# Kernel tuning notes

Hardware: AMD Instinct MI355X
Metric: run time of the kernel (lower is better)

The kernel has to match this reference:

```python
import jax, jax.numpy as jnp
import numpy as np


def setup_inputs() -> dict:
    key = jax.random.key(0)
    k1, k2, k3 = jax.random.split(key, 3)
    B, Cin, H, W = 64, 16, 256, 256
    Cout, K = 64, 3
    x = jax.random.normal(k1, (B, Cin, H, W), dtype=jnp.float32)
    # PyTorch Conv2d init scale ~ 1/sqrt(fan_in)
    fan_in = Cin * K * K
    conv_weight = jax.random.normal(k2, (Cout, Cin, K, K), dtype=jnp.float32) / np.sqrt(fan_in)
    conv_bias = jax.random.normal(k3, (Cout,), dtype=jnp.float32) / np.sqrt(fan_in)
    return {"x": x, "conv_weight": conv_weight, "conv_bias": conv_bias}


def reference(x, conv_weight, conv_bias):
    # Conv2d: stride=1, padding=0 (VALID), dilation=1, groups=1
    y = jax.lax.conv_general_dilated(
        x, conv_weight,
        window_strides=(1, 1),
        padding="VALID",
        dimension_numbers=("NCHW", "OIHW", "NCHW"),
    ) + conv_bias[None, :, None, None]          # [B, Cout, 254, 254]
    m = jnp.min(y, axis=1, keepdims=True)        # [B, 1, 254, 254] min over channels
    return jnp.tanh(jnp.tanh(m))                 # double tanh
```

## Files before the change

### kernel.cpp

```cpp
#include <hip/hip_runtime.h>
#include <math.h>

#define CIN    16
#define COUT   64
#define H      256
#define W      256
#define OH     254
#define OW     254
#define NTAP   9
#define RING   8
#define SROW   264
#define NIT    32

typedef _Float16 f16x8  __attribute__((ext_vector_type(8)));
typedef float    f32x16 __attribute__((ext_vector_type(16)));

#define XP(px) ((px) ^ (((px) >> 3) & 7))

__global__ void wpack_kernel(const float* __restrict__ w, _Float16* __restrict__ wpk) {
    int idx = blockIdx.x * 256 + threadIdx.x;
    if (idx >= NTAP * 2 * 64 * 8) return;
    int e = idx & 7, l = (idx >> 3) & 63, m = (idx >> 9) & 1, t = idx >> 10;
    int co  = (l & 31) + 32 * m;
    int cin = 8 * (l >> 5) + e;
    wpk[idx] = (_Float16)w[((co * CIN + cin) * 3 + t / 3) * 3 + (t % 3)];
}

__device__ __forceinline__ float tanh_fast(float v) {
    float e = __expf(2.0f * v);
    return 1.0f - 2.0f * __builtin_amdgcn_rcpf(e + 1.0f);
}
__device__ __forceinline__ float min3f(float a, float b, float c) {
    return fminf(fminf(a, b), c);
}

__global__ __launch_bounds__(256, 2) void conv_mfma_kernel(
        const float* __restrict__ x, const f16x8* __restrict__ wpk,
        const float* __restrict__ bias, float* __restrict__ out) {
    __shared__ f16x8 xs[RING * SROW];

    const int tid  = threadIdx.x;
    const int lane = tid & 63;

    int bid = blockIdx.x;
    int nb  = (bid & 7) * 64 + (bid >> 3);
    int b   = nb >> 3;
    int rem = nb & 7;
    const int P0 = (rem & 1) * 128;
    const int r0 = (rem >> 1) * 64;

    const float* xb = x + (size_t)b * CIN * H * W;

    f16x8 wreg[NTAP][2];
#pragma unroll
    for (int t = 0; t < NTAP; ++t)
#pragma unroll
        for (int m = 0; m < 2; ++m)
            wreg[t][m] = wpk[(t * 2 + m) * 64 + lane];

    const int wave = tid >> 6;
    const int l31  = lane & 31;
    const int g2   = lane >> 5;

    const int sr = tid >> 7;
    const int sg = (tid >> 6) & 1;
    const int sp = tid & 63;
    const bool hduty = (sp == 63);

    float2 vm[8];
    float2 vh[8];

#define SLOAD(dRel)                                                             \
    {                                                                           \
        int row_ = r0 + (dRel); if (row_ > 255) row_ = 255;                     \
        const float* p_ = xb + (size_t)row_ * W;                                \
        _Pragma("unroll")                                                       \
        for (int c = 0; c < 8; ++c)                                             \
            vm[c] = *(const float2*)(p_ + (size_t)(8 * sg + c) * (H * W) + P0 + 2 * sp); \
        if (hduty) {                                                            \
            int hp_ = P0 + 128; if (hp_ > 254) hp_ = 254;                       \
            _Pragma("unroll")                                                   \
            for (int c = 0; c < 8; ++c)                                         \
                vh[c] = *(const float2*)(p_ + (size_t)(8 * sg + c) * (H * W) + hp_); \
        }                                                                       \
    }

#define SWRITE(slot)                                                            \
    {                                                                           \
        f16x8 q0, q1;                                                           \
        _Pragma("unroll")                                                       \
        for (int c = 0; c < 8; ++c) { q0[c] = (_Float16)vm[c].x;                \
                                      q1[c] = (_Float16)vm[c].y; }              \
        f16x8* base_ = xs + (slot) * SROW + sg * 132;                           \
        base_[XP(2 * sp)]     = q0;                                             \
        base_[XP(2 * sp + 1)] = q1;                                             \
        if (hduty) {                                                            \
            f16x8 h0, h1;                                                       \
            _Pragma("unroll")                                                   \
            for (int c = 0; c < 8; ++c) { h0[c] = (_Float16)vh[c].x;            \
                                          h1[c] = (_Float16)vh[c].y; }          \
            base_[XP(128)] = h0;                                                \
            base_[XP(129)] = h1;                                                \
        }                                                                       \
    }

#pragma unroll
    for (int j = 0; j < 3; ++j) {
        SLOAD(2 * j + sr)
        SWRITE(2 * j + sr)
    }

    int roff[3];
#pragma unroll
    for (int kw = 0; kw < 3; ++kw)
        roff[kw] = g2 * 132 + XP(32 * wave + l31 + kw);

    f32x16 cbias[2];
#pragma unroll
    for (int m = 0; m < 2; ++m)
#pragma unroll
        for (int r = 0; r < 16; ++r)
            cbias[m][r] = bias[(r & 3) + 8 * (r >> 2) + 4 * g2 + 32 * m];

    __syncthreads();

#pragma unroll 1
    for (int i = 0; i < NIT; ++i) {
        const bool pf = (i < 30);
        if (pf) SLOAD(2 * i + 6 + sr)

        f32x16 acc[2][2];
#pragma unroll
        for (int dd = 0; dd < 4; ++dd) {
            const f16x8* xr = xs + ((2 * i + dd) & 7) * SROW;
            f16x8 f0 = xr[roff[0]];
            f16x8 f1 = xr[roff[1]];
            f16x8 f2 = xr[roff[2]];
#pragma unroll
            for (int ro = 0; ro < 2; ++ro) {
                const int kh = dd - ro;
                if (kh < 0 || kh > 2) continue;
#pragma unroll
                for (int m = 0; m < 2; ++m) {
                    if (kh == 0)
                        acc[ro][m] = __builtin_amdgcn_mfma_f32_32x32x16_f16(wreg[0][m], f0, cbias[m], 0, 0, 0);
                    else
                        acc[ro][m] = __builtin_amdgcn_mfma_f32_32x32x16_f16(wreg[kh * 3][m], f0, acc[ro][m], 0, 0, 0);
                    acc[ro][m] = __builtin_amdgcn_mfma_f32_32x32x16_f16(wreg[kh * 3 + 1][m], f1, acc[ro][m], 0, 0, 0);
                    acc[ro][m] = __builtin_amdgcn_mfma_f32_32x32x16_f16(wreg[kh * 3 + 2][m], f2, acc[ro][m], 0, 0, 0);
                }
            }
        }

        __syncthreads();
        if (pf) SWRITE((2 * i + 6 + sr) & 7)

#pragma unroll
        for (int ro = 0; ro < 2; ++ro) {
            const int oh = r0 + 2 * i + ro;
            float mn = fminf(acc[ro][0][0], acc[ro][1][0]);
#pragma unroll
            for (int q = 1; q < 16; ++q)
                mn = min3f(acc[ro][0][q], acc[ro][1][q], mn);
            mn = fminf(mn, __shfl_xor(mn, 32));
            float t2 = tanh_fast(tanh_fast(mn));
            const int px = P0 + 32 * wave + l31;
            if (g2 == 0 && px < OW && oh < OH)
                out[((size_t)b * OH + oh) * OW + px] = t2;
        }
    }
}

extern "C" void kernel_launch(void* const* d_in, const int* in_sizes, int n_in,
                              void* d_out, int out_size, void* d_ws, size_t ws_size,
                              hipStream_t stream) {
    const float* x    = (const float*)d_in[0];
    const float* w    = (const float*)d_in[1];
    const float* bias = (const float*)d_in[2];
    float* out = (float*)d_out;
    _Float16* wpk = (_Float16*)d_ws;

    wpack_kernel<<<36, 256, 0, stream>>>(w, wpk);
    conv_mfma_kernel<<<512, 256, 0, stream>>>(x, (const f16x8*)wpk, bias, out);
}
```

Baseline: 97.14 us.

## Replace row-streaming ring buffer with full-tile LDS staging and smaller blocks

Each block now loads an entire 18-row input tile (with halo) into shared memory up front and computes 16 output rows with no per-iteration barriers, instead of streaming 64 rows through an 8-slot ring. The grid grows fourfold and column tiles overlap so the right tile starts at column 124. This removes the in-loop sync and prefetch bookkeeping but increases halo reloads, uses more LDS per block, drops the bank-conflict swizzle, and loses overlap of loads with compute within a block.

```diff
diff --git a/kernel.cpp b/kernel.cpp
--- a/kernel.cpp
+++ b/kernel.cpp
@@ -1,21 +1,20 @@
 #include <hip/hip_runtime.h>
 #include <math.h>
 
-#define CIN    16
-#define COUT   64
-#define H      256
-#define W      256
-#define OH     254
-#define OW     254
-#define NTAP   9
-#define RING   8
-#define SROW   264
-#define NIT    32
+#define CIN   16
+#define COUT  64
+#define H     256
+#define W     256
+#define OH    254
+#define OW    254
+#define NTAP  9
+#define TROWS 16
+#define IROWS 18
+#define SROW  264
+#define HWSZ  (H * W)
 
 typedef _Float16 f16x8  __attribute__((ext_vector_type(8)));
 typedef float    f32x16 __attribute__((ext_vector_type(16)));
-
-#define XP(px) ((px) ^ (((px) >> 3) & 7))
 
 __global__ void wpack_kernel(const float* __restrict__ w, _Float16* __restrict__ wpk) {
     int idx = blockIdx.x * 256 + threadIdx.x;
@@ -37,19 +36,22 @@
 __global__ __launch_bounds__(256, 2) void conv_mfma_kernel(
         const float* __restrict__ x, const f16x8* __restrict__ wpk,
         const float* __restrict__ bias, float* __restrict__ out) {
-    __shared__ f16x8 xs[RING * SROW];
+    __shared__ f16x8 xs[IROWS * SROW];
 
     const int tid  = threadIdx.x;
     const int lane = tid & 63;
 
     int bid = blockIdx.x;
-    int nb  = (bid & 7) * 64 + (bid >> 3);
-    int b   = nb >> 3;
-    int rem = nb & 7;
-    const int P0 = (rem & 1) * 128;
-    const int r0 = (rem >> 1) * 64;
-
-    const float* xb = x + (size_t)b * CIN * H * W;
+    int nb  = (bid & 7) * 256 + (bid >> 3);
+    const int b    = nb >> 5;
+    const int rem  = nb & 31;
+    const int v    = rem >> 1;
+    const int col  = rem & 1;
+    const int r0   = v * TROWS;
+    const int base = col ? 124 : 0;
+    const int P0   = col * 128;
+
+    const float* xb = x + (size_t)b * CIN * HWSZ;
 
     f16x8 wreg[NTAP][2];
 #pragma unroll
@@ -57,63 +59,97 @@
 #pragma unroll
         for (int m = 0; m < 2; ++m)
             wreg[t][m] = wpk[(t * 2 + m) * 64 + lane];
+
+    float2 vA[8], vB[8];
+
+#define LOADU(k, vv)                                                            \
+    {                                                                           \
+        const int u_ = tid + 256 * (k);                                         \
+        const int row_ = u_ >> 7;                                               \
+        const int gq_  = (u_ >> 6) & 1;                                         \
+        const int p_   = u_ & 63;                                               \
+        int grow_ = r0 + row_; if (grow_ > 255) grow_ = 255;                    \
+        const float* gp_ = xb + (size_t)gq_ * 8 * HWSZ + (size_t)grow_ * W      \
+                              + base + 2 * p_;                                  \
+        _Pragma("unroll")                                                       \
+        for (int c = 0; c < 8; ++c) vv[c] = *(const float2*)(gp_ + (size_t)c * HWSZ); \
+    }                                                                           \
+    __builtin_amdgcn_sched_barrier(0);
+
+#define WRITEU(k, vv)                                                           \
+    {                                                                           \
+        const int u_ = tid + 256 * (k);                                         \
+        const int row_ = u_ >> 7;                                               \
+        const int gq_  = (u_ >> 6) & 1;                                         \
+        const int p_   = u_ & 63;                                               \
+        f16x8 q0_, q1_;                                                         \
+        _Pragma("unroll")                                                       \
+        for (int c = 0; c < 8; ++c) { q0_[c] = (_Float16)vv[c].x;               \
+                                      q1_[c] = (_Float16)vv[c].y; }             \
+        const int sl_ = row_ * SROW + gq_ * 132 + 2 * p_;                       \
+        xs[sl_]     = q0_;                                                      \
+        xs[sl_ + 1] = q1_;                                                      \
+    }
+
+#define LOADH(vv)                                                               \
+    if (tid < 72) {                                                             \
+        const int row_ = tid >> 2;                                              \
+        const int gq_  = (tid >> 1) & 1;                                        \
+        const int pp_  = tid & 1;                                               \
+        int grow_ = r0 + row_; if (grow_ > 255) grow_ = 255;                    \
+        const float* gp_ = xb + (size_t)gq_ * 8 * HWSZ + (size_t)grow_ * W      \
+                              + base + 128 + 2 * pp_;                           \
+        _Pragma("unroll")                                                       \
+        for (int c = 0; c < 8; ++c) vv[c] = *(const float2*)(gp_ + (size_t)c * HWSZ); \
+    }                                                                           \
+    __builtin_amdgcn_sched_barrier(0);
+
+#define WRITEH(vv)                                                              \
+    if (tid < 72) {                                                             \
+        const int row_ = tid >> 2;                                              \
+        const int gq_  = (tid >> 1) & 1;                                        \
+        const int pp_  = tid & 1;                                               \
+        f16x8 q0_, q1_;                                                         \
+        _Pragma("unroll")                                                       \
+        for (int c = 0; c < 8; ++c) { q0_[c] = (_Float16)vv[c].x;               \
+                                      q1_[c] = (_Float16)vv[c].y; }             \
+        const int sl_ = row_ * SROW + gq_ * 132 + 128 + 2 * pp_;                \
+        xs[sl_]     = q0_;                                                      \
+        xs[sl_ + 1] = q1_;                                                      \
+    }
+
+    LOADU(0, vA)
+    LOADU(1, vB)
+    WRITEU(0, vA)
+    LOADU(2, vA)
+    WRITEU(1, vB)
+    LOADU(3, vB)
+    WRITEU(2, vA)
+    LOADU(4, vA)
+    WRITEU(3, vB)
+    LOADU(5, vB)
+    WRITEU(4, vA)
+    LOADU(6, vA)
+    WRITEU(5, vB)
+    LOADU(7, vB)
+    WRITEU(6, vA)
+    LOADU(8, vA)
+    WRITEU(7, vB)
+    LOADH(vB)
+    WRITEU(8, vA)
+    WRITEH(vB)
 
     const int wave = tid >> 6;
     const int l31  = lane & 31;
     const int g2   = lane >> 5;
 
-    const int sr = tid >> 7;
-    const int sg = (tid >> 6) & 1;
-    const int sp = tid & 63;
-    const bool hduty = (sp == 63);
-
-    float2 vm[8];
-    float2 vh[8];
-
-#define SLOAD(dRel)                                                             \
-    {                                                                           \
-        int row_ = r0 + (dRel); if (row_ > 255) row_ = 255;                     \
-        const float* p_ = xb + (size_t)row_ * W;                                \
-        _Pragma("unroll")                                                       \
-        for (int c = 0; c < 8; ++c)                                             \
-            vm[c] = *(const float2*)(p_ + (size_t)(8 * sg + c) * (H * W) + P0 + 2 * sp); \
-        if (hduty) {                                                            \
-            int hp_ = P0 + 128; if (hp_ > 254) hp_ = 254;                       \
-            _Pragma("unroll")                                                   \
-            for (int c = 0; c < 8; ++c)                                         \
-                vh[c] = *(const float2*)(p_ + (size_t)(8 * sg + c) * (H * W) + hp_); \
-        }                                                                       \
-    }
-
-#define SWRITE(slot)                                                            \
-    {                                                                           \
-        f16x8 q0, q1;                                                           \
-        _Pragma("unroll")                                                       \
-        for (int c = 0; c < 8; ++c) { q0[c] = (_Float16)vm[c].x;                \
-                                      q1[c] = (_Float16)vm[c].y; }              \
-        f16x8* base_ = xs + (slot) * SROW + sg * 132;                           \
-        base_[XP(2 * sp)]     = q0;                                             \
-        base_[XP(2 * sp + 1)] = q1;                                             \
-        if (hduty) {                                                            \
-            f16x8 h0, h1;                                                       \
-            _Pragma("unroll")                                                   \
-            for (int c = 0; c < 8; ++c) { h0[c] = (_Float16)vh[c].x;            \
-                                          h1[c] = (_Float16)vh[c].y; }          \
-            base_[XP(128)] = h0;                                                \
-            base_[XP(129)] = h1;                                                \
-        }                                                                       \
-    }
-
-#pragma unroll
-    for (int j = 0; j < 3; ++j) {
-        SLOAD(2 * j + sr)
-        SWRITE(2 * j + sr)
-    }
-
     int roff[3];
 #pragma unroll
-    for (int kw = 0; kw < 3; ++kw)
-        roff[kw] = g2 * 132 + XP(32 * wave + l31 + kw);
+    for (int kw = 0; kw < 3; ++kw) {
+        int lp = (col ? 4 : 0) + 32 * wave + l31 + kw;
+        if (lp > 131) lp = 131;
+        roff[kw] = g2 * 132 + lp;
+    }
 
     f32x16 cbias[2];
 #pragma unroll
@@ -125,14 +161,11 @@
     __syncthreads();
 
 #pragma unroll 1
-    for (int i = 0; i < NIT; ++i) {
-        const bool pf = (i < 30);
-        if (pf) SLOAD(2 * i + 6 + sr)
-
+    for (int i = 0; i < TROWS / 2; ++i) {
         f32x16 acc[2][2];
 #pragma unroll
         for (int dd = 0; dd < 4; ++dd) {
-            const f16x8* xr = xs + ((2 * i + dd) & 7) * SROW;
+            const f16x8* xr = xs + (2 * i + dd) * SROW;
             f16x8 f0 = xr[roff[0]];
             f16x8 f1 = xr[roff[1]];
             f16x8 f2 = xr[roff[2]];
@@ -152,9 +185,6 @@
             }
         }
 
-        __syncthreads();
-        if (pf) SWRITE((2 * i + 6 + sr) & 7)
-
 #pragma unroll
         for (int ro = 0; ro < 2; ++ro) {
             const int oh = r0 + 2 * i + ro;
@@ -181,5 +211,5 @@
     _Float16* wpk = (_Float16*)d_ws;
 
     wpack_kernel<<<36, 256, 0, stream>>>(w, wpk);
-    conv_mfma_kernel<<<512, 256, 0, stream>>>(x, (const f16x8*)wpk, bias, out);
-}
+    conv_mfma_kernel<<<2048, 256, 0, stream>>>(x, (const f16x8*)wpk, bias, out);
+}
```

Measured after the change: 91.27 us. 6.0% less time.

## Restructure conv into 512-thread blocks with double-buffered 8-row tiles

Applied to the files above, without the earlier changes.

Switches from 256-thread blocks with an 8-slot ring of 2 rows per iteration to 512-thread blocks that double-buffer 10-row input tiles and produce 8 output rows per tile. Wave pairs split the rows and the grid is halved. The column halves now start at 124 instead of 128 so the halo comes from the main load, and the XOR swizzle is dropped. The goal is fewer barriers per output row and more load/compute overlap. The cost is more LDS per block, possible bank conflicts without the swizzle, and some threads idle during the tile load.

```diff
diff --git a/kernel.cpp b/kernel.cpp
--- a/kernel.cpp
+++ b/kernel.cpp
@@ -1,21 +1,22 @@
 #include <hip/hip_runtime.h>
 #include <math.h>
 
-#define CIN    16
-#define COUT   64
-#define H      256
-#define W      256
-#define OH     254
-#define OW     254
-#define NTAP   9
-#define RING   8
-#define SROW   264
-#define NIT    32
+#define CIN   16
+#define COUT  64
+#define H     256
+#define W     256
+#define OH    254
+#define OW    254
+#define NTAP  9
+#define HWSZ  (H * W)
+#define TOR   8
+#define TIR   10
+#define SROW  264
+#define BUFS  (TIR * SROW)
+#define NTILE 16
 
 typedef _Float16 f16x8  __attribute__((ext_vector_type(8)));
 typedef float    f32x16 __attribute__((ext_vector_type(16)));
-
-#define XP(px) ((px) ^ (((px) >> 3) & 7))
 
 __global__ void wpack_kernel(const float* __restrict__ w, _Float16* __restrict__ wpk) {
     int idx = blockIdx.x * 256 + threadIdx.x;
@@ -34,22 +35,24 @@
     return fminf(fminf(a, b), c);
 }
 
-__global__ __launch_bounds__(256, 2) void conv_mfma_kernel(
+__global__ __launch_bounds__(512, 2) void conv_mfma_kernel(
         const float* __restrict__ x, const f16x8* __restrict__ wpk,
         const float* __restrict__ bias, float* __restrict__ out) {
-    __shared__ f16x8 xs[RING * SROW];
+    __shared__ f16x8 xs[2][BUFS];
 
     const int tid  = threadIdx.x;
     const int lane = tid & 63;
 
     int bid = blockIdx.x;
-    int nb  = (bid & 7) * 64 + (bid >> 3);
-    int b   = nb >> 3;
-    int rem = nb & 7;
-    const int P0 = (rem & 1) * 128;
-    const int r0 = (rem >> 1) * 64;
-
-    const float* xb = x + (size_t)b * CIN * H * W;
+    int nb  = (bid & 7) * 32 + (bid >> 3);
+    const int img  = nb >> 2;
+    const int half = (nb >> 1) & 1;
+    const int col  = nb & 1;
+    const int base = col * 124;
+    const int P0   = col * 128;
+    const int R0   = half * 128;
+
+    const float* xb = x + (size_t)img * CIN * HWSZ;
 
     f16x8 wreg[NTAP][2];
 #pragma unroll
@@ -58,62 +61,60 @@
         for (int m = 0; m < 2; ++m)
             wreg[t][m] = wpk[(t * 2 + m) * 64 + lane];
 
-    const int wave = tid >> 6;
-    const int l31  = lane & 31;
-    const int g2   = lane >> 5;
-
-    const int sr = tid >> 7;
-    const int sg = (tid >> 6) & 1;
-    const int sp = tid & 63;
-    const bool hduty = (sp == 63);
-
-    float2 vm[8];
-    float2 vh[8];
-
-#define SLOAD(dRel)                                                             \
+    int row_[3], g_[3], pp_[3];
+#pragma unroll
+    for (int k = 0; k < 3; ++k) {
+        int u = tid + 512 * k;
+        row_[k] = u / 132;
+        int rem = u - 132 * row_[k];
+        g_[k]  = (rem >= 66) ? 1 : 0;
+        pp_[k] = rem - 66 * g_[k];
+    }
+    const bool act2 = (tid < 296);
+
+#define SLOADK(k, rbase, vv)                                                    \
     {                                                                           \
-        int row_ = r0 + (dRel); if (row_ > 255) row_ = 255;                     \
-        const float* p_ = xb + (size_t)row_ * W;                                \
+        int grow = (rbase) + row_[k]; if (grow > 255) grow = 255;               \
+        const float* gp = xb + (size_t)g_[k] * 8 * HWSZ + (size_t)grow * W      \
+                             + base + 2 * pp_[k];                               \
         _Pragma("unroll")                                                       \
-        for (int c = 0; c < 8; ++c)                                             \
-            vm[c] = *(const float2*)(p_ + (size_t)(8 * sg + c) * (H * W) + P0 + 2 * sp); \
-        if (hduty) {                                                            \
-            int hp_ = P0 + 128; if (hp_ > 254) hp_ = 254;                       \
-            _Pragma("unroll")                                                   \
-            for (int c = 0; c < 8; ++c)                                         \
-                vh[c] = *(const float2*)(p_ + (size_t)(8 * sg + c) * (H * W) + hp_); \
-        }                                                                       \
-    }
-
-#define SWRITE(slot)                                                            \
+        for (int c = 0; c < 8; ++c) vv[c] = *(const float2*)(gp + (size_t)c * HWSZ); \
+    }
+
+#define SWRITEK(k, bufp, vv)                                                    \
     {                                                                           \
         f16x8 q0, q1;                                                           \
         _Pragma("unroll")                                                       \
-        for (int c = 0; c < 8; ++c) { q0[c] = (_Float16)vm[c].x;                \
-                                      q1[c] = (_Float16)vm[c].y; }              \
-        f16x8* base_ = xs + (slot) * SROW + sg * 132;                           \
-        base_[XP(2 * sp)]     = q0;                                             \
-        base_[XP(2 * sp + 1)] = q1;                                             \
-        if (hduty) {                                                            \
-            f16x8 h0, h1;                                                       \
-            _Pragma("unroll")                                                   \
-            for (int c = 0; c < 8; ++c) { h0[c] = (_Float16)vh[c].x;            \
-                                          h1[c] = (_Float16)vh[c].y; }          \
-            base_[XP(128)] = h0;                                                \
-            base_[XP(129)] = h1;                                                \
-        }                                                                       \
-    }
-
-#pragma unroll
-    for (int j = 0; j < 3; ++j) {
-        SLOAD(2 * j + sr)
-        SWRITE(2 * j + sr)
-    }
+        for (int c = 0; c < 8; ++c) { q0[c] = (_Float16)vv[c].x;                \
+                                      q1[c] = (_Float16)vv[c].y; }              \
+        int sl_ = row_[k] * SROW + g_[k] * 132 + 2 * pp_[k];                    \
+        (bufp)[sl_]     = q0;                                                   \
+        (bufp)[sl_ + 1] = q1;                                                   \
+    }
+
+    {
+        float2 v0[8], v1[8], v2[8];
+        SLOADK(0, R0, v0)
+        SLOADK(1, R0, v1)
+        if (act2) SLOADK(2, R0, v2)
+        SWRITEK(0, xs[0], v0)
+        SWRITEK(1, xs[0], v1)
+        if (act2) SWRITEK(2, xs[0], v2)
+    }
+
+    const int wave = tid >> 6;
+    const int pr   = wave >> 2;
+    const int sl4  = wave & 3;
+    const int l31  = lane & 31;
+    const int g2   = lane >> 5;
 
     int roff[3];
 #pragma unroll
-    for (int kw = 0; kw < 3; ++kw)
-        roff[kw] = g2 * 132 + XP(32 * wave + l31 + kw);
+    for (int kw = 0; kw < 3; ++kw) {
+        int lp = (col ? 4 : 0) + 32 * sl4 + l31 + kw;
+        if (lp > 131) lp = 131;
+        roff[kw] = g2 * 132 + lp;
+    }
 
     f32x16 cbias[2];
 #pragma unroll
@@ -124,50 +125,72 @@
 
     __syncthreads();
 
+    float2 vA[8], vB[8], vC[8];
+    int cur = 0;
+
 #pragma unroll 1
-    for (int i = 0; i < NIT; ++i) {
-        const bool pf = (i < 30);
-        if (pf) SLOAD(2 * i + 6 + sr)
-
-        f32x16 acc[2][2];
-#pragma unroll
-        for (int dd = 0; dd < 4; ++dd) {
-            const f16x8* xr = xs + ((2 * i + dd) & 7) * SROW;
-            f16x8 f0 = xr[roff[0]];
-            f16x8 f1 = xr[roff[1]];
-            f16x8 f2 = xr[roff[2]];
-#pragma unroll
-            for (int ro = 0; ro < 2; ++ro) {
-                const int kh = dd - ro;
-                if (kh < 0 || kh > 2) continue;
-#pragma unroll
-                for (int m = 0; m < 2; ++m) {
-                    if (kh == 0)
-                        acc[ro][m] = __builtin_amdgcn_mfma_f32_32x32x16_f16(wreg[0][m], f0, cbias[m], 0, 0, 0);
-                    else
-                        acc[ro][m] = __builtin_amdgcn_mfma_f32_32x32x16_f16(wreg[kh * 3][m], f0, acc[ro][m], 0, 0, 0);
-                    acc[ro][m] = __builtin_amdgcn_mfma_f32_32x32x16_f16(wreg[kh * 3 + 1][m], f1, acc[ro][m], 0, 0, 0);
-                    acc[ro][m] = __builtin_amdgcn_mfma_f32_32x32x16_f16(wreg[kh * 3 + 2][m], f2, acc[ro][m], 0, 0, 0);
+    for (int t = 0; t < NTILE; ++t) {
+        const int r0 = R0 + t * TOR;
+        const bool pf = (t + 1 < NTILE);
+
+        if (pf) {
+            const int rn = r0 + TOR;
+            SLOADK(0, rn, vA)
+            SLOADK(1, rn, vB)
+            if (act2) SLOADK(2, rn, vC)
+        }
+        __builtin_amdgcn_sched_barrier(0);
+
+        const f16x8* bufc = &xs[cur][0];
+
+#pragma unroll
+        for (int i = 0; i < 2; ++i) {
+            f32x16 acc[2][2];
+#pragma unroll
+            for (int dd = 0; dd < 4; ++dd) {
+                const f16x8* xr = bufc + (4 * i + 2 * pr + dd) * SROW;
+                f16x8 f0 = xr[roff[0]];
+                f16x8 f1 = xr[roff[1]];
+                f16x8 f2 = xr[roff[2]];
+#pragma unroll
+                for (int ro = 0; ro < 2; ++ro) {
+                    const int kh = dd - ro;
+                    if (kh < 0 || kh > 2) continue;
+#pragma unroll
+                    for (int m = 0; m < 2; ++m) {
+                        if (kh == 0)
+                            acc[ro][m] = __builtin_amdgcn_mfma_f32_32x32x16_f16(wreg[0][m], f0, cbias[m], 0, 0, 0);
+                        else
+                            acc[ro][m] = __builtin_amdgcn_mfma_f32_32x32x16_f16(wreg[kh * 3][m], f0, acc[ro][m], 0, 0, 0);
+                        acc[ro][m] = __builtin_amdgcn_mfma_f32_32x32x16_f16(wreg[kh * 3 + 1][m], f1, acc[ro][m], 0, 0, 0);
+                        acc[ro][m] = __builtin_amdgcn_mfma_f32_32x32x16_f16(wreg[kh * 3 + 2][m], f2, acc[ro][m], 0, 0, 0);
+                    }
                 }
             }
+#pragma unroll
+            for (int ro = 0; ro < 2; ++ro) {
+                const int oh = r0 + 4 * i + 2 * pr + ro;
+                float mn = fminf(acc[ro][0][0], acc[ro][1][0]);
+#pragma unroll
+                for (int q = 1; q < 16; ++q)
+                    mn = min3f(acc[ro][0][q], acc[ro][1][q], mn);
+                mn = fminf(mn, __shfl_xor(mn, 32));
+                float t2 = tanh_fast(tanh_fast(mn));
+                const int px = P0 + 32 * sl4 + l31;
+                if (g2 == 0 && px < OW && oh < OH)
+                    out[((size_t)img * OH + oh) * OW + px] = t2;
+            }
         }
-
+        __builtin_amdgcn_sched_barrier(0);
+
+        if (pf) {
+            f16x8* bufn = &xs[cur ^ 1][0];
+            SWRITEK(0, bufn, vA)
+            SWRITEK(1, bufn, vB)
+            if (act2) SWRITEK(2, bufn, vC)
+        }
         __syncthreads();
-        if (pf) SWRITE((2 * i + 6 + sr) & 7)
-
-#pragma unroll
-        for (int ro = 0; ro < 2; ++ro) {
-            const int oh = r0 + 2 * i + ro;
-            float mn = fminf(acc[ro][0][0], acc[ro][1][0]);
-#pragma unroll
-            for (int q = 1; q < 16; ++q)
-                mn = min3f(acc[ro][0][q], acc[ro][1][q], mn);
-            mn = fminf(mn, __shfl_xor(mn, 32));
-            float t2 = tanh_fast(tanh_fast(mn));
-            const int px = P0 + 32 * wave + l31;
-            if (g2 == 0 && px < OW && oh < OH)
-                out[((size_t)b * OH + oh) * OW + px] = t2;
-        }
+        cur ^= 1;
     }
 }
 
@@ -181,5 +204,5 @@
     _Float16* wpk = (_Float16*)d_ws;
 
     wpack_kernel<<<36, 256, 0, stream>>>(w, wpk);
-    conv_mfma_kernel<<<512, 256, 0, stream>>>(x, (const f16x8*)wpk, bias, out);
-}
+    conv_mfma_kernel<<<256, 512, 0, stream>>>(x, (const f16x8*)wpk, bias, out);
+}
```

After: 110.1 us. +13.3%, slower.
